# Kernel tuning notes

Measured on AMD Instinct MI355X. Metric: run time of the kernel, lower is better.

The kernel has to match this reference:

```python
import jax, jax.numpy as jnp
import numpy as np

DIM, PATCHES, HID, NCLS, NBLK, PS = 384, 196, 1536, 1000, 24, 16

def fq(w, bits=8):
    # symmetric per-tensor fake quantization (dequantized), as in QAT DynamicQLinear
    n = float(2 ** (bits - 1) - 1)
    s = jnp.max(jnp.abs(w)) / n + 1e-8
    q = jnp.clip(jnp.round(w / s), -n - 1.0, n) * s
    return q

def setup_inputs() -> dict:
    key = jax.random.key(0)
    ks = jax.random.split(key, 12)
    d = {}
    d["x"] = jax.random.normal(ks[0], (64, 3, 224, 224), jnp.float32)
    d["conv_w"] = jax.random.normal(ks[1], (DIM, 3, PS, PS), jnp.float32) * 0.02
    d["conv_b"] = jnp.zeros((DIM,), jnp.float32)
    d["norm1_a"] = jnp.ones((NBLK, DIM), jnp.float32)
    d["norm1_b"] = jnp.zeros((NBLK, DIM), jnp.float32)
    d["attn_w"] = jax.random.normal(ks[2], (NBLK, PATCHES, PATCHES), jnp.float32) * 0.02
    d["attn_b"] = jnp.zeros((NBLK, PATCHES), jnp.float32)
    d["gamma1"] = jnp.full((NBLK, DIM), 1e-4, jnp.float32)
    d["norm2_a"] = jnp.ones((NBLK, DIM), jnp.float32)
    d["norm2_b"] = jnp.zeros((NBLK, DIM), jnp.float32)
    d["mlp_w1"] = jax.random.normal(ks[3], (NBLK, HID, DIM), jnp.float32) * 0.02
    d["mlp_b1"] = jnp.zeros((NBLK, HID), jnp.float32)
    d["mlp_w2"] = jax.random.normal(ks[4], (NBLK, DIM, HID), jnp.float32) * 0.02
    d["mlp_b2"] = jnp.zeros((NBLK, DIM), jnp.float32)
    d["gamma2"] = jnp.full((NBLK, DIM), 1e-4, jnp.float32)
    d["norm_a"] = jnp.ones((DIM,), jnp.float32)
    d["norm_b"] = jnp.zeros((DIM,), jnp.float32)
    d["head_w"] = jax.random.normal(ks[5], (NCLS, DIM), jnp.float32) * 0.02
    d["head_b"] = jnp.zeros((NCLS,), jnp.float32)
    return d

def reference(x, conv_w, conv_b, norm1_a, norm1_b, attn_w, attn_b, gamma1,
              norm2_a, norm2_b, mlp_w1, mlp_b1, mlp_w2, mlp_b2, gamma2,
              norm_a, norm_b, head_w, head_b):
    B = x.shape[0]
    # patch embed: quantized 16x16 stride-16 conv, then flatten(2).transpose(1,2)
    h = jax.lax.conv_general_dilated(x, fq(conv_w), (PS, PS), 'VALID',
                                     dimension_numbers=('NCHW', 'OIHW', 'NCHW'))
    h = h + conv_b[None, :, None, None]
    h = h.reshape(B, DIM, PATCHES).transpose(0, 2, 1)  # [B, 196, 384]

    def step(xc, p):
        a1, b1, aw, ab, g1, a2, b2, w1, bb1, w2, bb2, g2 = p
        # affine norm1 (per-channel)
        t = xc * a1 + b1
        # cross-patch linear applied on transposed layout: out[b,q,d] = sum_p t[b,p,d] W[q,p]
        t = jnp.einsum('bpd,qp->bqd', t, fq(aw)) + ab[None, :, None]
        xc = g1 * t + xc
        # affine norm2 + MLP (384 -> 1536 -> 384, exact GELU)
        t = xc * a2 + b2
        t = jax.nn.gelu(jnp.einsum('bpd,hd->bph', t, fq(w1)) + bb1, approximate=False)
        t = jnp.einsum('bph,dh->bpd', t, fq(w2)) + bb2
        xc = g2 * t + xc
        return xc, None

    h, _ = jax.lax.scan(step, h, (norm1_a, norm1_b, attn_w, attn_b, gamma1,
                                  norm2_a, norm2_b, mlp_w1, mlp_b1, mlp_w2, mlp_b2, gamma2))
    h = h * norm_a + norm_b          # final affine norm
    h = h.mean(axis=1)               # mean pool over patches -> [B, 384]
    return h @ fq(head_w).T + head_b  # [B, 1000]
```

## Files before the change

kernel.cpp:

```cpp
#include <hip/hip_runtime.h>

#define DIM 384
#define PATCHES 196
#define HID 1536
#define NBLK 24
#define NPAD 256
#define XROWS (64 * PATCHES)
#define BDCOLS (64 * DIM)
#define XELEMS (XROWS * DIM)
#define ESTRIDE 132

typedef __attribute__((ext_vector_type(8))) short s8v;
typedef __attribute__((ext_vector_type(4))) float f4v;
typedef unsigned char uchar;
typedef long long i64t;

__device__ __forceinline__ short f2bf(float f) {
  unsigned u = __float_as_uint(f);
  u += 0x7FFFu + ((u >> 16) & 1u);
  return (short)(u >> 16);
}

__device__ __forceinline__ float gelu_f(float x) {
  float u2 = 1.5957691216f * (x + 0.044715f * x * x * x);
  return x / (1.0f + __expf(-u2));
}

__device__ __forceinline__ unsigned pk4_fp8(float a, float b, float c, float d) {
  int lo = __builtin_amdgcn_cvt_pk_fp8_f32(a, b, 0, false);
  int full = __builtin_amdgcn_cvt_pk_fp8_f32(c, d, lo, true);
  return (unsigned)full;
}
__device__ __forceinline__ uchar fp8_1(float a) {
  return (uchar)(__builtin_amdgcn_cvt_pk_fp8_f32(a, a, 0, false) & 0xff);
}

__device__ __forceinline__ void gload_lds16(const void* g, void* l) {
  __builtin_amdgcn_global_load_lds((const __attribute__((address_space(1))) void*)g,
                                   (__attribute__((address_space(3))) void*)l, 16, 0, 0);
}

__global__ __launch_bounds__(256)
void absmax_v4(const float* __restrict__ src, int f4per, int blocks_per,
               unsigned* __restrict__ out) {
  int tens = blockIdx.x / blocks_per;
  int sl = blockIdx.x - tens * blocks_per;
  const float4* p = (const float4*)(src + (size_t)tens * f4per * 4);
  float m = 0.f;
  for (int i = sl * 256 + threadIdx.x; i < f4per; i += blocks_per * 256) {
    float4 v = p[i];
    m = fmaxf(m, fmaxf(fmaxf(fabsf(v.x), fabsf(v.y)), fmaxf(fabsf(v.z), fabsf(v.w))));
  }
  __shared__ float red[256];
  red[threadIdx.x] = m;
  __syncthreads();
  for (int s = 128; s > 0; s >>= 1) {
    if ((int)threadIdx.x < s) red[threadIdx.x] = fmaxf(red[threadIdx.x], red[threadIdx.x + s]);
    __syncthreads();
  }
  if (threadIdx.x == 0) atomicMax(out + tens, __float_as_uint(red[0]));
}

__global__ __launch_bounds__(256)
void quant_w(const float* __restrict__ w, short* __restrict__ q,
             const unsigned* __restrict__ sc, int per, int total) {
  int i = blockIdx.x * 256 + threadIdx.x;
  if (i >= total) return;
  int tens = i / per;
  float s = __uint_as_float(sc[tens]) / 127.0f + 1e-8f;
  float v = rintf(w[i] / s);
  v = fminf(fmaxf(v, -128.0f), 127.0f) * s;
  q[i] = f2bf(v);
}

__global__ __launch_bounds__(256)
void quant_fp8(const float* __restrict__ w, unsigned* __restrict__ q,
               const unsigned* __restrict__ sc, int per, int total4) {
  int i = blockIdx.x * 256 + threadIdx.x;
  if (i >= total4) return;
  int e = i << 2;
  int tens = e / per;
  float s = __uint_as_float(sc[tens]) / 127.0f + 1e-8f;
  float4 w4 = *(const float4*)(w + e);
  float a = fminf(fmaxf(rintf(w4.x / s), -128.0f), 127.0f) * s;
  float b = fminf(fmaxf(rintf(w4.y / s), -128.0f), 127.0f) * s;
  float c = fminf(fmaxf(rintf(w4.z / s), -128.0f), 127.0f) * s;
  float d = fminf(fmaxf(rintf(w4.w / s), -128.0f), 127.0f) * s;
  q[i] = pk4_fp8(a, b, c, d);
}

__global__ __launch_bounds__(256)
void quant_attn_fp8(const float* __restrict__ w, unsigned* __restrict__ q,
                    const unsigned* __restrict__ sc) {
  int i = blockIdx.x * 256 + threadIdx.x;
  if (i >= NBLK * PATCHES * NPAD / 4) return;
  int e = i << 2;
  int col = e & (NPAD - 1);
  int rt = e >> 8;
  int row = rt % PATCHES;
  int tens = rt / PATCHES;
  float s = __uint_as_float(sc[tens]) / 127.0f + 1e-8f;
  const float* wr = w + (size_t)tens * PATCHES * PATCHES + (size_t)row * PATCHES;
  float v[4];
#pragma unroll
  for (int k = 0; k < 4; ++k) {
    int c = col + k;
    v[k] = (c < PATCHES) ? fminf(fmaxf(rintf(wr[c] / s), -128.0f), 127.0f) * s : 0.f;
  }
  q[i] = pk4_fp8(v[0], v[1], v[2], v[3]);
}

__global__ __launch_bounds__(256)
void quant_head_v4(const float* __restrict__ w, float* __restrict__ q,
                   const unsigned* __restrict__ sc) {
  int i = blockIdx.x * 256 + threadIdx.x;
  if (i >= 1000 * DIM / 4) return;
  float s = __uint_as_float(sc[0]) / 127.0f + 1e-8f;
  float4 w4 = *(const float4*)(w + (i << 2));
  float4 o;
  o.x = fminf(fmaxf(rintf(w4.x / s), -128.0f), 127.0f) * s;
  o.y = fminf(fmaxf(rintf(w4.y / s), -128.0f), 127.0f) * s;
  o.z = fminf(fmaxf(rintf(w4.z / s), -128.0f), 127.0f) * s;
  o.w = fminf(fmaxf(rintf(w4.w / s), -128.0f), 127.0f) * s;
  *(float4*)(q + (i << 2)) = o;
}

__global__ __launch_bounds__(256)
void im2col_k(const float* __restrict__ x, short* __restrict__ Xa) {
  int idx = blockIdx.x * 256 + threadIdx.x;
  if (idx >= XROWS * 768 / 4) return;
  int e = idx << 2;
  int r = e / 768, k = e - r * 768;
  int b = r / PATCHES, p = r - b * PATCHES;
  int c = k >> 8, rem = k & 255, ii = rem >> 4, j = rem & 15;
  int ph = p / 14, pw = p - ph * 14;
  const float4 v = *(const float4*)(x + (b * 3 + c) * 50176 + (ph * 16 + ii) * 224 + pw * 16 + j);
  short2* o = (short2*)(Xa + e);
  o[0] = make_short2(f2bf(v.x), f2bf(v.y));
  o[1] = make_short2(f2bf(v.z), f2bf(v.w));
}

__global__ __launch_bounds__(256)
void gemm_conv(const short* __restrict__ A, const short* __restrict__ B,
               float* __restrict__ Xres, const float* __restrict__ bias,
               const float* __restrict__ n1a, const float* __restrict__ n1b,
               uchar* __restrict__ Yt) {
  constexpr int TILE_SHORTS = 192 * 64;
  __shared__ char smem[2 * TILE_SHORTS * 2];
  short* buf0 = (short*)smem;
  float* S = (float*)smem;
  const int lda = 768, K = 768;

  const int t = threadIdx.x;
  const int lane = t & 63;
  const int wid = t >> 6;
  const int wr = wid >> 1, wc = wid & 1;

  const int gx = gridDim.x;
  const int nwg = gx * gridDim.y;
  const int orig = blockIdx.y * gx + blockIdx.x;
  const int q = nwg >> 3, rm = nwg & 7;
  const int xc = orig & 7, jj = orig >> 3;
  const int wg = (xc < rm ? xc * (q + 1) : rm * (q + 1) + (xc - rm) * q) + jj;
  const int bx = wg % gx, by = wg / gx;
  const int m0 = by * 64, n0 = bx * 128;

  f4v acc[2][4];
#pragma unroll
  for (int m = 0; m < 2; ++m)
#pragma unroll
    for (int n = 0; n < 4; ++n) acc[m][n] = (f4v){0.f, 0.f, 0.f, 0.f};

  const int srow = t >> 3;
  const int scol = ((t & 7) ^ (srow & 7)) << 3;
  const short* ga[2];
#pragma unroll
  for (int h = 0; h < 2; ++h) ga[h] = A + (size_t)(m0 + h * 32 + srow) * lda + scol;
  const short* gb[4];
#pragma unroll
  for (int j = 0; j < 4; ++j) gb[j] = B + (size_t)(n0 + j * 32 + srow) * lda + scol;
  short* ldst = buf0 + (t & ~63) * 8;

  auto stage = [&](int slot, int kt) {
    const int koff = kt << 6;
    const int boff = slot * TILE_SHORTS;
    gload_lds16(ga[0] + koff, ldst + boff);
    gload_lds16(ga[1] + koff, ldst + boff + 2048);
#pragma unroll
    for (int j = 0; j < 4; ++j)
      gload_lds16(gb[j] + koff, ldst + boff + 4096 + j * 2048);
  };

  const int l15 = lane & 15, lk = lane >> 4, l7 = lane & 7;
  int paoff[2], pboff[2];
#pragma unroll
  for (int ks = 0; ks < 2; ++ks) {
    const int cgx = ((ks << 2) + lk) ^ l7;
    paoff[ks] = (wr * 32 + l15) * 64 + (cgx << 3);
    pboff[ks] = 4096 + (wc * 64 + l15) * 64 + (cgx << 3);
  }

  const int nk = K >> 6;
  stage(0, 0);
  asm volatile("s_waitcnt vmcnt(0)" ::: "memory");
  __builtin_amdgcn_s_barrier();
  for (int kt = 0; kt < nk; ++kt) {
    const int cur = kt & 1;
    if (kt + 1 < nk) stage(cur ^ 1, kt + 1);
    const short* base = buf0 + cur * TILE_SHORTS;
    s8v af[2][2], bfr[4][2];
#pragma unroll
    for (int m = 0; m < 2; ++m)
#pragma unroll
      for (int ks = 0; ks < 2; ++ks) af[m][ks] = *(const s8v*)(base + paoff[ks] + m * 1024);
#pragma unroll
    for (int n = 0; n < 4; ++n)
#pragma unroll
      for (int ks = 0; ks < 2; ++ks) bfr[n][ks] = *(const s8v*)(base + pboff[ks] + n * 1024);
    asm volatile("s_waitcnt lgkmcnt(0)" ::: "memory");
    __builtin_amdgcn_sched_barrier(0);
    __builtin_amdgcn_s_setprio(1);
#pragma unroll
    for (int m = 0; m < 2; ++m)
#pragma unroll
      for (int n = 0; n < 4; ++n)
#pragma unroll
        for (int ks = 0; ks < 2; ++ks)
          acc[m][n] = __builtin_amdgcn_mfma_f32_16x16x32_bf16(af[m][ks], bfr[n][ks], acc[m][n], 0, 0, 0);
    __builtin_amdgcn_s_setprio(0);
    if (kt + 1 < nk) {
      asm volatile("s_waitcnt vmcnt(0)" ::: "memory");
      __builtin_amdgcn_s_barrier();
    }
  }

  const int cb = (wc << 6) + l15;
  const int rl = t >> 3;
  const int c0 = (t & 7) << 4;
#pragma unroll
  for (int m = 0; m < 2; ++m) {
    __syncthreads();
#pragma unroll
    for (int n = 0; n < 4; ++n) {
      int c = cb + n * 16;
#pragma unroll
      for (int j = 0; j < 4; ++j)
        S[((wr << 4) + (lk << 2) + j) * ESTRIDE + c] = acc[m][n][j];
    }
    __syncthreads();
    const int r = m0 + (rl >> 4) * 32 + m * 16 + (rl & 15);
    const int colg = n0 + c0;
    float xn[16];
#pragma unroll
    for (int i = 0; i < 4; ++i) {
      float4 q4 = *(const float4*)(S + rl * ESTRIDE + c0 + i * 4);
      float4 b4 = *(const float4*)(bias + colg + i * 4);
      float4 o4 = make_float4(q4.x + b4.x, q4.y + b4.y, q4.z + b4.z, q4.w + b4.w);
      *(float4*)(Xres + (size_t)r * DIM + colg + i * 4) = o4;
      xn[4 * i] = o4.x; xn[4 * i + 1] = o4.y; xn[4 * i + 2] = o4.z; xn[4 * i + 3] = o4.w;
    }
    int bb = r / PATCHES, p = r - bb * PATCHES;
    uchar* yrow = Yt + ((size_t)(bb * DIM + colg)) * NPAD + p;
#pragma unroll
    for (int i = 0; i < 4; ++i) {
      float4 a4 = *(const float4*)(n1a + colg + i * 4);
      float4 b4 = *(const float4*)(n1b + colg + i * 4);
      yrow[(4 * i + 0) * NPAD] = fp8_1(xn[4 * i] * a4.x + b4.x);
      yrow[(4 * i + 1) * NPAD] = fp8_1(xn[4 * i + 1] * a4.y + b4.y);
      yrow[(4 * i + 2) * NPAD] = fp8_1(xn[4 * i + 2] * a4.z + b4.z);
      yrow[(4 * i + 3) * NPAD] = fp8_1(xn[4 * i + 3] * a4.w + b4.w);
    }
  }
}

template <int EPI>
__global__ __launch_bounds__(256)
void gemm8(const uchar* __restrict__ A, int lda8, int Mlim,
           const uchar* __restrict__ B, int ldb8, int K,
           float* __restrict__ Xres, uchar* __restrict__ OutB8,
           const float* __restrict__ bias, const float* __restrict__ gamma,
           const float* __restrict__ n2a, const float* __restrict__ n2b,
           const float* __restrict__ n1a, const float* __restrict__ n1b,
           uchar* __restrict__ Yt) {
  constexpr int TILE_BYTES = 192 * 128;
  __shared__ char smem[2 * TILE_BYTES];
  char* buf0 = smem;
  float* S = (float*)smem;

  const int t = threadIdx.x;
  const int lane = t & 63;
  const int wid = t >> 6;
  const int wr = wid >> 1, wc = wid & 1;

  const int gx = gridDim.x;
  const int nwg = gx * gridDim.y;
  const int orig = blockIdx.y * gx + blockIdx.x;
  const int q = nwg >> 3, rm = nwg & 7;
  const int xc = orig & 7, jj = orig >> 3;
  const int wg = (xc < rm ? xc * (q + 1) : rm * (q + 1) + (xc - rm) * q) + jj;
  const int bx = wg % gx, by = wg / gx;
  const int m0 = by * 64, n0 = bx * 128;

  f4v acc[2][4];
#pragma unroll
  for (int m = 0; m < 2; ++m)
#pragma unroll
    for (int n = 0; n < 4; ++n) acc[m][n] = (f4v){0.f, 0.f, 0.f, 0.f};

  const int srow = t >> 3;
  const int scolB = (((t & 7) ^ (srow & 7)) << 4);
  const uchar* ga[2];
#pragma unroll
  for (int h = 0; h < 2; ++h) {
    int r = m0 + h * 32 + srow;
    if (r >= Mlim) r = Mlim - 1;
    ga[h] = A + (size_t)r * lda8 + scolB;
  }
  const uchar* gb[4];
#pragma unroll
  for (int j = 0; j < 4; ++j)
    gb[j] = B + (size_t)(n0 + j * 32 + srow) * ldb8 + scolB;
  char* ldst = buf0 + (t & ~63) * 16;

  auto stage = [&](int slot, int kt) {
    const int koff = kt << 7;
    const int boff = slot * TILE_BYTES;
    gload_lds16(ga[0] + koff, ldst + boff);
    gload_lds16(ga[1] + koff, ldst + boff + 4096);
#pragma unroll
    for (int j = 0; j < 4; ++j)
      gload_lds16(gb[j] + koff, ldst + boff + 8192 + j * 4096);
  };

  const int l15 = lane & 15, lk = lane >> 4, l7 = lane & 7;
  int cterm[4];
#pragma unroll
  for (int ks = 0; ks < 4; ++ks)
    cterm[ks] = ((((ks << 1) + (lk >> 1)) ^ l7) << 4) + ((lk & 1) << 3);
  int arow[2], brow[4];
#pragma unroll
  for (int m = 0; m < 2; ++m) arow[m] = (wr * 32 + m * 16 + l15) << 7;
#pragma unroll
  for (int n = 0; n < 4; ++n) brow[n] = 8192 + ((wc * 64 + n * 16 + l15) << 7);

  const int nk = K >> 7;
  stage(0, 0);
  asm volatile("s_waitcnt vmcnt(0)" ::: "memory");
  __builtin_amdgcn_s_barrier();
  for (int kt = 0; kt < nk; ++kt) {
    const int cur = kt & 1;
    if (kt + 1 < nk) stage(cur ^ 1, kt + 1);
    const char* base = buf0 + cur * TILE_BYTES;
    i64t af[2][4], bfr[4][4];
#pragma unroll
    for (int m = 0; m < 2; ++m)
#pragma unroll
      for (int ks = 0; ks < 4; ++ks) af[m][ks] = *(const i64t*)(base + arow[m] + cterm[ks]);
#pragma unroll
    for (int n = 0; n < 4; ++n)
#pragma unroll
      for (int ks = 0; ks < 4; ++ks) bfr[n][ks] = *(const i64t*)(base + brow[n] + cterm[ks]);
    asm volatile("s_waitcnt lgkmcnt(0)" ::: "memory");
    __builtin_amdgcn_sched_barrier(0);
    __builtin_amdgcn_s_setprio(1);
#pragma unroll
    for (int ks = 0; ks < 4; ++ks)
#pragma unroll
      for (int m = 0; m < 2; ++m)
#pragma unroll
        for (int n = 0; n < 4; ++n)
          acc[m][n] = __builtin_amdgcn_mfma_f32_16x16x32_fp8_fp8(af[m][ks], bfr[n][ks], acc[m][n], 0, 0, 0);
    __builtin_amdgcn_s_setprio(0);
    if (kt + 1 < nk) {
      asm volatile("s_waitcnt vmcnt(0)" ::: "memory");
      __builtin_amdgcn_s_barrier();
    }
  }

  const int cb = (wc << 6) + l15;
  const int rl = t >> 3;
  const int c0 = (t & 7) << 4;
#pragma unroll
  for (int m = 0; m < 2; ++m) {
    __syncthreads();
#pragma unroll
    for (int n = 0; n < 4; ++n) {
      int c = cb + n * 16;
#pragma unroll
      for (int j = 0; j < 4; ++j)
        S[((wr << 4) + (lk << 2) + j) * ESTRIDE + c] = acc[m][n][j];
    }
    __syncthreads();
    const int r = m0 + (rl >> 4) * 32 + m * 16 + (rl & 15);
    const int colg = n0 + c0;
    float v[16];
#pragma unroll
    for (int i = 0; i < 4; ++i) {
      float4 q4 = *(const float4*)(S + rl * ESTRIDE + c0 + i * 4);
      v[4 * i] = q4.x; v[4 * i + 1] = q4.y; v[4 * i + 2] = q4.z; v[4 * i + 3] = q4.w;
    }
    if (EPI == 1) {
      if (r < Mlim) {
        const int b = colg / DIM, d0 = colg - b * DIM;
        const float br = bias[r];
        const size_t base2 = (size_t)b * (PATCHES * DIM) + (size_t)r * DIM + d0;
        float xn[16];
#pragma unroll
        for (int i = 0; i < 4; ++i) {
          float4 g4 = *(const float4*)(gamma + d0 + i * 4);
          float4 x4 = *(const float4*)(Xres + base2 + i * 4);
          x4.x += g4.x * (v[4 * i] + br);
          x4.y += g4.y * (v[4 * i + 1] + br);
          x4.z += g4.z * (v[4 * i + 2] + br);
          x4.w += g4.w * (v[4 * i + 3] + br);
          *(float4*)(Xres + base2 + i * 4) = x4;
          xn[4 * i] = x4.x; xn[4 * i + 1] = x4.y; xn[4 * i + 2] = x4.z; xn[4 * i + 3] = x4.w;
        }
        unsigned o[4];
#pragma unroll
        for (int i = 0; i < 4; ++i) {
          float4 a4 = *(const float4*)(n2a + d0 + i * 4);
          float4 b4 = *(const float4*)(n2b + d0 + i * 4);
          o[i] = pk4_fp8(xn[4 * i] * a4.x + b4.x, xn[4 * i + 1] * a4.y + b4.y,
                         xn[4 * i + 2] * a4.z + b4.z, xn[4 * i + 3] * a4.w + b4.w);
        }
        *(uint4*)(OutB8 + base2) = make_uint4(o[0], o[1], o[2], o[3]);
      }
    } else if (EPI == 2) {
      unsigned o[4];
#pragma unroll
      for (int i = 0; i < 4; ++i) {
        float g0 = gelu_f(v[4 * i] + bias[colg + 4 * i]);
        float g1 = gelu_f(v[4 * i + 1] + bias[colg + 4 * i + 1]);
        float g2 = gelu_f(v[4 * i + 2] + bias[colg + 4 * i + 2]);
        float g3 = gelu_f(v[4 * i + 3] + bias[colg + 4 * i + 3]);
        o[i] = pk4_fp8(g0, g1, g2, g3);
      }
      *(uint4*)(OutB8 + (size_t)r * HID + colg) = make_uint4(o[0], o[1], o[2], o[3]);
    } else {
      float xn[16];
#pragma unroll
      for (int i = 0; i < 4; ++i) {
        float4 b4 = *(const float4*)(bias + colg + i * 4);
        float4 g4 = *(const float4*)(gamma + colg + i * 4);
        float4 x4 = *(const float4*)(Xres + (size_t)r * DIM + colg + i * 4);
        x4.x += g4.x * (v[4 * i] + b4.x);
        x4.y += g4.y * (v[4 * i + 1] + b4.y);
        x4.z += g4.z * (v[4 * i + 2] + b4.z);
        x4.w += g4.w * (v[4 * i + 3] + b4.w);
        *(float4*)(Xres + (size_t)r * DIM + colg + i * 4) = x4;
        xn[4 * i] = x4.x; xn[4 * i + 1] = x4.y; xn[4 * i + 2] = x4.z; xn[4 * i + 3] = x4.w;
      }
      if (Yt != nullptr) {
        int bb = r / PATCHES, p = r - bb * PATCHES;
        uchar* yrow = Yt + ((size_t)(bb * DIM + colg)) * NPAD + p;
#pragma unroll
        for (int i = 0; i < 4; ++i) {
          float4 a4 = *(const float4*)(n1a + colg + i * 4);
          float4 b4 = *(const float4*)(n1b + colg + i * 4);
          yrow[(4 * i + 0) * NPAD] = fp8_1(xn[4 * i] * a4.x + b4.x);
          yrow[(4 * i + 1) * NPAD] = fp8_1(xn[4 * i + 1] * a4.y + b4.y);
          yrow[(4 * i + 2) * NPAD] = fp8_1(xn[4 * i + 2] * a4.z + b4.z);
          yrow[(4 * i + 3) * NPAD] = fp8_1(xn[4 * i + 3] * a4.w + b4.w);
        }
      }
    }
  }
}

__global__ __launch_bounds__(256)
void poolnorm2(const float* __restrict__ X, const float* __restrict__ na,
               const float* __restrict__ nb, float* __restrict__ pooled) {
  __shared__ float red[4][64];
  const int b = blockIdx.x, d0 = blockIdx.y * 64;
  const int dl = threadIdx.x & 63, g = threadIdx.x >> 6;
  const float* p = X + (size_t)b * (PATCHES * DIM) + d0 + dl;
  float s = 0.f;
  for (int i = g; i < PATCHES; i += 4) s += p[(size_t)i * DIM];
  red[g][dl] = s;
  __syncthreads();
  if (threadIdx.x < 64) {
    float tot = red[0][dl] + red[1][dl] + red[2][dl] + red[3][dl];
    int d = d0 + dl;
    pooled[b * DIM + d] = (tot * (1.0f / 196.0f)) * na[d] + nb[d];
  }
}

__global__ __launch_bounds__(256)
void head_k2(const float* __restrict__ pooled, const float* __restrict__ Whq,
             const float* __restrict__ hb, float* __restrict__ out) {
  __shared__ float pl[DIM];
  const int b = blockIdx.x, t = threadIdx.x;
  if (t < 192) {
    pl[t] = pooled[b * DIM + t];
    pl[t + 192] = pooled[b * DIM + t + 192];
  }
  __syncthreads();
  const int n = blockIdx.y * 64 + (t >> 2);
  if (n >= 1000) return;
  const int qofs = (t & 3) * 96;
  const float4* w = (const float4*)(Whq + (size_t)n * DIM + qofs);
  const float* p = pl + qofs;
  float s = 0.f;
#pragma unroll 6
  for (int i = 0; i < 24; ++i) {
    float4 wv = w[i];
    s += p[4 * i] * wv.x + p[4 * i + 1] * wv.y + p[4 * i + 2] * wv.z + p[4 * i + 3] * wv.w;
  }
  s += __shfl_down(s, 2, 4);
  s += __shfl_down(s, 1, 4);
  if ((t & 3) == 0) out[b * 1000 + n] = s + hb[n];
}

extern "C" void kernel_launch(void* const* d_in, const int* in_sizes, int n_in,
                              void* d_out, int out_size, void* d_ws, size_t ws_size,
                              hipStream_t stream) {
  const float* x       = (const float*)d_in[0];
  const float* conv_w  = (const float*)d_in[1];
  const float* conv_b  = (const float*)d_in[2];
  const float* norm1_a = (const float*)d_in[3];
  const float* norm1_b = (const float*)d_in[4];
  const float* attn_w  = (const float*)d_in[5];
  const float* attn_b  = (const float*)d_in[6];
  const float* gamma1  = (const float*)d_in[7];
  const float* norm2_a = (const float*)d_in[8];
  const float* norm2_b = (const float*)d_in[9];
  const float* mlp_w1  = (const float*)d_in[10];
  const float* mlp_b1  = (const float*)d_in[11];
  const float* mlp_w2  = (const float*)d_in[12];
  const float* mlp_b2  = (const float*)d_in[13];
  const float* gamma2  = (const float*)d_in[14];
  const float* norm_a  = (const float*)d_in[15];
  const float* norm_b  = (const float*)d_in[16];
  const float* head_w  = (const float*)d_in[17];
  const float* head_b  = (const float*)d_in[18];
  (void)in_sizes; (void)n_in; (void)out_size; (void)ws_size;

  char* ws = (char*)d_ws;
  size_t off = 0;
  auto alloc = [&](size_t bytes) {
    off = (off + 255) & ~(size_t)255;
    void* p = ws + off;
    off += bytes;
    return p;
  };
  unsigned* scales = (unsigned*)alloc(74 * 4);
  short* conv_wq = (short*)alloc((size_t)DIM * 768 * 2);
  uchar* attn_wq = (uchar*)alloc((size_t)NBLK * PATCHES * NPAD);
  uchar* w1q     = (uchar*)alloc((size_t)NBLK * HID * DIM);
  uchar* w2q     = (uchar*)alloc((size_t)NBLK * DIM * HID);
  float* headq   = (float*)alloc((size_t)1000 * DIM * 4);
  float* X       = (float*)alloc((size_t)XELEMS * 4);
  uchar* Yt      = (uchar*)alloc((size_t)BDCOLS * NPAD);
  uchar* Y2      = (uchar*)alloc((size_t)XELEMS);
  uchar* H       = (uchar*)alloc((size_t)XROWS * HID);
  float* pooled  = (float*)alloc((size_t)64 * DIM * 4);
  short* Xa = (short*)H;

  hipMemsetAsync(scales, 0, 74 * 4, stream);
  hipMemsetAsync(Yt, 0, (size_t)BDCOLS * NPAD, stream);
  absmax_v4<<<32, 256, 0, stream>>>(conv_w, DIM * 768 / 4, 32, scales + 0);
  absmax_v4<<<32, 256, 0, stream>>>(head_w, 1000 * DIM / 4, 32, scales + 1);
  absmax_v4<<<NBLK * 8, 256, 0, stream>>>(attn_w, PATCHES * PATCHES / 4, 8, scales + 2);
  absmax_v4<<<NBLK * 64, 256, 0, stream>>>(mlp_w1, HID * DIM / 4, 64, scales + 26);
  absmax_v4<<<NBLK * 64, 256, 0, stream>>>(mlp_w2, DIM * HID / 4, 64, scales + 50);

  quant_w<<<(DIM * 768 + 255) / 256, 256, 0, stream>>>(conv_w, conv_wq, scales + 0, DIM * 768, DIM * 768);
  quant_fp8<<<(NBLK * HID * DIM / 4 + 255) / 256, 256, 0, stream>>>(
      mlp_w1, (unsigned*)w1q, scales + 26, HID * DIM, NBLK * HID * DIM / 4);
  quant_fp8<<<(NBLK * HID * DIM / 4 + 255) / 256, 256, 0, stream>>>(
      mlp_w2, (unsigned*)w2q, scales + 50, DIM * HID, NBLK * DIM * HID / 4);
  quant_attn_fp8<<<(NBLK * PATCHES * NPAD / 4 + 255) / 256, 256, 0, stream>>>(
      attn_w, (unsigned*)attn_wq, scales + 2);
  quant_head_v4<<<(1000 * DIM / 4 + 255) / 256, 256, 0, stream>>>(head_w, headq, scales + 1);

  im2col_k<<<(XROWS * 768 / 4) / 256, 256, 0, stream>>>(x, Xa);
  gemm_conv<<<dim3(3, 196), 256, 0, stream>>>(Xa, conv_wq, X, conv_b, norm1_a, norm1_b, Yt);

  for (int blk = 0; blk < NBLK; ++blk) {
    gemm8<1><<<dim3(BDCOLS / 128, 4), 256, 0, stream>>>(
        attn_wq + (size_t)blk * PATCHES * NPAD, NPAD, PATCHES, Yt, NPAD, NPAD,
        X, Y2, attn_b + blk * PATCHES, gamma1 + blk * DIM,
        norm2_a + blk * DIM, norm2_b + blk * DIM, nullptr, nullptr, nullptr);
    gemm8<2><<<dim3(HID / 128, XROWS / 64), 256, 0, stream>>>(
        Y2, DIM, XROWS, w1q + (size_t)blk * HID * DIM, DIM, DIM,
        nullptr, H, mlp_b1 + blk * HID, nullptr, nullptr, nullptr,
        nullptr, nullptr, nullptr);
    const bool last = (blk == NBLK - 1);
    gemm8<3><<<dim3(DIM / 128, XROWS / 64), 256, 0, stream>>>(
        H, HID, XROWS, w2q + (size_t)blk * DIM * HID, HID, HID,
        X, nullptr, mlp_b2 + blk * DIM, gamma2 + blk * DIM, nullptr, nullptr,
        last ? nullptr : norm1_a + (blk + 1) * DIM,
        last ? nullptr : norm1_b + (blk + 1) * DIM,
        last ? nullptr : Yt);
  }

  poolnorm2<<<dim3(64, 6), 256, 0, stream>>>(X, norm_a, norm_b, pooled);
  head_k2<<<dim3(64, 16), 256, 0, stream>>>(pooled, headq, head_b, (float*)d_out);
}
```

Measured before the change: 2.130 ms.

## Halve K tile, prefetch two stages ahead, raise occupancy, vectorize epilogue stores

The fp8 GEMM K-tile shrinks from 128 to 64 bytes, which halves LDS use and lets launch_bounds request 4 workgroups per CU. The loop now keeps two stages in flight, waiting with vmcnt(3) instead of draining all loads before each tile. The epilogue stages one 32-row half at a time. The residual-update variant is remapped so each thread owns 4 consecutive patches and writes packed 4-byte fp8 stores into the transposed Yt buffer instead of single-byte scattered stores. The trade-offs are more barriers per K step and more register pressure under the tighter occupancy bound.

```diff
diff --git a/kernel.cpp b/kernel.cpp
--- a/kernel.cpp
+++ b/kernel.cpp
@@ -274,15 +274,15 @@
 }
 
 template <int EPI>
-__global__ __launch_bounds__(256)
-void gemm8(const uchar* __restrict__ A, int lda8, int Mlim,
+__global__ __launch_bounds__(256, 4)
+void gemmS(const uchar* __restrict__ A, int lda8, int Mlim,
            const uchar* __restrict__ B, int ldb8, int K,
            float* __restrict__ Xres, uchar* __restrict__ OutB8,
            const float* __restrict__ bias, const float* __restrict__ gamma,
            const float* __restrict__ n2a, const float* __restrict__ n2b,
            const float* __restrict__ n1a, const float* __restrict__ n1b,
            uchar* __restrict__ Yt) {
-  constexpr int TILE_BYTES = 192 * 128;
+  constexpr int TILE_BYTES = 192 * 64;
   __shared__ char smem[2 * TILE_BYTES];
   char* buf0 = smem;
   float* S = (float*)smem;
@@ -307,161 +307,164 @@
 #pragma unroll
     for (int n = 0; n < 4; ++n) acc[m][n] = (f4v){0.f, 0.f, 0.f, 0.f};
 
-  const int srow = t >> 3;
-  const int scolB = (((t & 7) ^ (srow & 7)) << 4);
-  const uchar* ga[2];
-#pragma unroll
-  for (int h = 0; h < 2; ++h) {
-    int r = m0 + h * 32 + srow;
-    if (r >= Mlim) r = Mlim - 1;
-    ga[h] = A + (size_t)r * lda8 + scolB;
-  }
-  const uchar* gb[4];
-#pragma unroll
-  for (int j = 0; j < 4; ++j)
-    gb[j] = B + (size_t)(n0 + j * 32 + srow) * ldb8 + scolB;
+  const int srow = t >> 2;
+  const int scolB = (((t & 3) ^ (srow & 3)) << 4);
+  int ra = m0 + srow;
+  if (ra >= Mlim) ra = Mlim - 1;
+  const uchar* ga = A + (size_t)ra * lda8 + scolB;
+  const uchar* gb[2];
+#pragma unroll
+  for (int j = 0; j < 2; ++j)
+    gb[j] = B + (size_t)(n0 + j * 64 + srow) * ldb8 + scolB;
   char* ldst = buf0 + (t & ~63) * 16;
 
   auto stage = [&](int slot, int kt) {
-    const int koff = kt << 7;
+    const int koff = kt << 6;
     const int boff = slot * TILE_BYTES;
-    gload_lds16(ga[0] + koff, ldst + boff);
-    gload_lds16(ga[1] + koff, ldst + boff + 4096);
-#pragma unroll
-    for (int j = 0; j < 4; ++j)
-      gload_lds16(gb[j] + koff, ldst + boff + 8192 + j * 4096);
+    gload_lds16(ga + koff, ldst + boff);
+    gload_lds16(gb[0] + koff, ldst + boff + 4096);
+    gload_lds16(gb[1] + koff, ldst + boff + 8192);
   };
 
-  const int l15 = lane & 15, lk = lane >> 4, l7 = lane & 7;
-  int cterm[4];
-#pragma unroll
-  for (int ks = 0; ks < 4; ++ks)
-    cterm[ks] = ((((ks << 1) + (lk >> 1)) ^ l7) << 4) + ((lk & 1) << 3);
+  const int l15 = lane & 15, lk = lane >> 4;
+  int cterm[2];
+#pragma unroll
+  for (int ks = 0; ks < 2; ++ks)
+    cterm[ks] = ((((ks << 1) + (lk >> 1)) ^ (l15 & 3)) << 4) + ((lk & 1) << 3);
   int arow[2], brow[4];
 #pragma unroll
-  for (int m = 0; m < 2; ++m) arow[m] = (wr * 32 + m * 16 + l15) << 7;
-#pragma unroll
-  for (int n = 0; n < 4; ++n) brow[n] = 8192 + ((wc * 64 + n * 16 + l15) << 7);
-
-  const int nk = K >> 7;
+  for (int m = 0; m < 2; ++m) arow[m] = (wr * 32 + m * 16 + l15) << 6;
+#pragma unroll
+  for (int n = 0; n < 4; ++n) brow[n] = 4096 + ((wc * 64 + n * 16 + l15) << 6);
+
+  const int nk = K >> 6;
   stage(0, 0);
-  asm volatile("s_waitcnt vmcnt(0)" ::: "memory");
-  __builtin_amdgcn_s_barrier();
+  if (nk > 1) stage(1, 1);
+  int cur = 0;
   for (int kt = 0; kt < nk; ++kt) {
-    const int cur = kt & 1;
-    if (kt + 1 < nk) stage(cur ^ 1, kt + 1);
+    if (kt + 1 < nk) { asm volatile("s_waitcnt vmcnt(3)" ::: "memory"); }
+    else             { asm volatile("s_waitcnt vmcnt(0)" ::: "memory"); }
+    __builtin_amdgcn_s_barrier();
     const char* base = buf0 + cur * TILE_BYTES;
-    i64t af[2][4], bfr[4][4];
+    i64t af[2][2], bfr[4][2];
 #pragma unroll
     for (int m = 0; m < 2; ++m)
 #pragma unroll
-      for (int ks = 0; ks < 4; ++ks) af[m][ks] = *(const i64t*)(base + arow[m] + cterm[ks]);
+      for (int ks = 0; ks < 2; ++ks) af[m][ks] = *(const i64t*)(base + arow[m] + cterm[ks]);
 #pragma unroll
     for (int n = 0; n < 4; ++n)
 #pragma unroll
-      for (int ks = 0; ks < 4; ++ks) bfr[n][ks] = *(const i64t*)(base + brow[n] + cterm[ks]);
+      for (int ks = 0; ks < 2; ++ks) bfr[n][ks] = *(const i64t*)(base + brow[n] + cterm[ks]);
     asm volatile("s_waitcnt lgkmcnt(0)" ::: "memory");
     __builtin_amdgcn_sched_barrier(0);
     __builtin_amdgcn_s_setprio(1);
 #pragma unroll
-    for (int ks = 0; ks < 4; ++ks)
+    for (int ks = 0; ks < 2; ++ks)
 #pragma unroll
       for (int m = 0; m < 2; ++m)
 #pragma unroll
         for (int n = 0; n < 4; ++n)
           acc[m][n] = __builtin_amdgcn_mfma_f32_16x16x32_fp8_fp8(af[m][ks], bfr[n][ks], acc[m][n], 0, 0, 0);
     __builtin_amdgcn_s_setprio(0);
-    if (kt + 1 < nk) {
-      asm volatile("s_waitcnt vmcnt(0)" ::: "memory");
-      __builtin_amdgcn_s_barrier();
-    }
-  }
-
-  const int cb = (wc << 6) + l15;
-  const int rl = t >> 3;
-  const int c0 = (t & 7) << 4;
-#pragma unroll
-  for (int m = 0; m < 2; ++m) {
+    __builtin_amdgcn_s_barrier();
+    if (kt + 2 < nk) stage(cur, kt + 2);
+    cur ^= 1;
+  }
+
+#pragma unroll
+  for (int hf = 0; hf < 2; ++hf) {
     __syncthreads();
-#pragma unroll
-    for (int n = 0; n < 4; ++n) {
-      int c = cb + n * 16;
-#pragma unroll
-      for (int j = 0; j < 4; ++j)
-        S[((wr << 4) + (lk << 2) + j) * ESTRIDE + c] = acc[m][n][j];
+    if (wr == hf) {
+#pragma unroll
+      for (int m = 0; m < 2; ++m)
+#pragma unroll
+        for (int n = 0; n < 4; ++n) {
+          int srow2 = m * 16 + (lk << 2);
+          int scol2 = wc * 64 + n * 16 + l15;
+#pragma unroll
+          for (int j = 0; j < 4; ++j)
+            S[(srow2 + j) * ESTRIDE + scol2] = acc[m][n][j];
+        }
     }
     __syncthreads();
-    const int r = m0 + (rl >> 4) * 32 + m * 16 + (rl & 15);
-    const int colg = n0 + c0;
-    float v[16];
-#pragma unroll
-    for (int i = 0; i < 4; ++i) {
-      float4 q4 = *(const float4*)(S + rl * ESTRIDE + c0 + i * 4);
-      v[4 * i] = q4.x; v[4 * i + 1] = q4.y; v[4 * i + 2] = q4.z; v[4 * i + 3] = q4.w;
-    }
-    if (EPI == 1) {
-      if (r < Mlim) {
-        const int b = colg / DIM, d0 = colg - b * DIM;
-        const float br = bias[r];
-        const size_t base2 = (size_t)b * (PATCHES * DIM) + (size_t)r * DIM + d0;
-        float xn[16];
+
+    if (EPI == 1 || EPI == 2) {
+      const int rl = t >> 3;
+      const int c0 = (t & 7) << 4;
+      const int r = m0 + hf * 32 + rl;
+      const int colg = n0 + c0;
+      float v[16];
+#pragma unroll
+      for (int i = 0; i < 4; ++i) {
+        float4 q4 = *(const float4*)(S + rl * ESTRIDE + c0 + i * 4);
+        v[4 * i] = q4.x; v[4 * i + 1] = q4.y; v[4 * i + 2] = q4.z; v[4 * i + 3] = q4.w;
+      }
+      if (EPI == 1) {
+        if (r < Mlim) {
+          const int b = colg / DIM, d0 = colg - b * DIM;
+          const float br = bias[r];
+          const size_t base2 = (size_t)b * (PATCHES * DIM) + (size_t)r * DIM + d0;
+          float xn[16];
+#pragma unroll
+          for (int i = 0; i < 4; ++i) {
+            float4 g4 = *(const float4*)(gamma + d0 + i * 4);
+            float4 x4 = *(const float4*)(Xres + base2 + i * 4);
+            x4.x += g4.x * (v[4 * i] + br);
+            x4.y += g4.y * (v[4 * i + 1] + br);
+            x4.z += g4.z * (v[4 * i + 2] + br);
+            x4.w += g4.w * (v[4 * i + 3] + br);
+            *(float4*)(Xres + base2 + i * 4) = x4;
+            xn[4 * i] = x4.x; xn[4 * i + 1] = x4.y; xn[4 * i + 2] = x4.z; xn[4 * i + 3] = x4.w;
+          }
+          unsigned o[4];
+#pragma unroll
+          for (int i = 0; i < 4; ++i) {
+            float4 a4 = *(const float4*)(n2a + d0 + i * 4);
+            float4 b4 = *(const float4*)(n2b + d0 + i * 4);
+            o[i] = pk4_fp8(xn[4 * i] * a4.x + b4.x, xn[4 * i + 1] * a4.y + b4.y,
+                           xn[4 * i + 2] * a4.z + b4.z, xn[4 * i + 3] * a4.w + b4.w);
+          }
+          *(uint4*)(OutB8 + base2) = make_uint4(o[0], o[1], o[2], o[3]);
+        }
+      } else {
+        unsigned o[4];
 #pragma unroll
         for (int i = 0; i < 4; ++i) {
-          float4 g4 = *(const float4*)(gamma + d0 + i * 4);
-          float4 x4 = *(const float4*)(Xres + base2 + i * 4);
-          x4.x += g4.x * (v[4 * i] + br);
-          x4.y += g4.y * (v[4 * i + 1] + br);
-          x4.z += g4.z * (v[4 * i + 2] + br);
-          x4.w += g4.w * (v[4 * i + 3] + br);
-          *(float4*)(Xres + base2 + i * 4) = x4;
-          xn[4 * i] = x4.x; xn[4 * i + 1] = x4.y; xn[4 * i + 2] = x4.z; xn[4 * i + 3] = x4.w;
+          float4 b4 = *(const float4*)(bias + colg + i * 4);
+          o[i] = pk4_fp8(gelu_f(v[4 * i] + b4.x), gelu_f(v[4 * i + 1] + b4.y),
+                         gelu_f(v[4 * i + 2] + b4.z), gelu_f(v[4 * i + 3] + b4.w));
         }
-        unsigned o[4];
-#pragma unroll
-        for (int i = 0; i < 4; ++i) {
-          float4 a4 = *(const float4*)(n2a + d0 + i * 4);
-          float4 b4 = *(const float4*)(n2b + d0 + i * 4);
-          o[i] = pk4_fp8(xn[4 * i] * a4.x + b4.x, xn[4 * i + 1] * a4.y + b4.y,
-                         xn[4 * i + 2] * a4.z + b4.z, xn[4 * i + 3] * a4.w + b4.w);
-        }
-        *(uint4*)(OutB8 + base2) = make_uint4(o[0], o[1], o[2], o[3]);
+        *(uint4*)(OutB8 + (size_t)r * HID + colg) = make_uint4(o[0], o[1], o[2], o[3]);
       }
-    } else if (EPI == 2) {
-      unsigned o[4];
-#pragma unroll
-      for (int i = 0; i < 4; ++i) {
-        float g0 = gelu_f(v[4 * i] + bias[colg + 4 * i]);
-        float g1 = gelu_f(v[4 * i + 1] + bias[colg + 4 * i + 1]);
-        float g2 = gelu_f(v[4 * i + 2] + bias[colg + 4 * i + 2]);
-        float g3 = gelu_f(v[4 * i + 3] + bias[colg + 4 * i + 3]);
-        o[i] = pk4_fp8(g0, g1, g2, g3);
-      }
-      *(uint4*)(OutB8 + (size_t)r * HID + colg) = make_uint4(o[0], o[1], o[2], o[3]);
     } else {
-      float xn[16];
-#pragma unroll
-      for (int i = 0; i < 4; ++i) {
-        float4 b4 = *(const float4*)(bias + colg + i * 4);
-        float4 g4 = *(const float4*)(gamma + colg + i * 4);
-        float4 x4 = *(const float4*)(Xres + (size_t)r * DIM + colg + i * 4);
-        x4.x += g4.x * (v[4 * i] + b4.x);
-        x4.y += g4.y * (v[4 * i + 1] + b4.y);
-        x4.z += g4.z * (v[4 * i + 2] + b4.z);
-        x4.w += g4.w * (v[4 * i + 3] + b4.w);
-        *(float4*)(Xres + (size_t)r * DIM + colg + i * 4) = x4;
-        xn[4 * i] = x4.x; xn[4 * i + 1] = x4.y; xn[4 * i + 2] = x4.z; xn[4 * i + 3] = x4.w;
+      const int r0 = m0 + hf * 32 + ((t & 7) << 2);
+      const int colg = n0 + ((t >> 3) << 2);
+      float4 b4 = *(const float4*)(bias + colg);
+      float4 g4 = *(const float4*)(gamma + colg);
+      float xn[4][4];
+#pragma unroll
+      for (int j = 0; j < 4; ++j) {
+        const int rloc = ((t & 7) << 2) + j;
+        float4 q0 = *(const float4*)(S + rloc * ESTRIDE + (colg - n0));
+        float* xp = Xres + (size_t)(r0 + j) * DIM + colg;
+        float4 x0 = *(const float4*)xp;
+        x0.x += g4.x * (q0.x + b4.x); x0.y += g4.y * (q0.y + b4.y);
+        x0.z += g4.z * (q0.z + b4.z); x0.w += g4.w * (q0.w + b4.w);
+        *(float4*)xp = x0;
+        xn[j][0] = x0.x; xn[j][1] = x0.y; xn[j][2] = x0.z; xn[j][3] = x0.w;
       }
       if (Yt != nullptr) {
-        int bb = r / PATCHES, p = r - bb * PATCHES;
-        uchar* yrow = Yt + ((size_t)(bb * DIM + colg)) * NPAD + p;
+        const int bb = r0 / PATCHES;
+        const int p0 = r0 - bb * PATCHES;
+        float4 a4 = *(const float4*)(n1a + colg);
+        float4 bv4 = *(const float4*)(n1b + colg);
+        float a[4] = {a4.x, a4.y, a4.z, a4.w};
+        float bv[4] = {bv4.x, bv4.y, bv4.z, bv4.w};
 #pragma unroll
         for (int i = 0; i < 4; ++i) {
-          float4 a4 = *(const float4*)(n1a + colg + i * 4);
-          float4 b4 = *(const float4*)(n1b + colg + i * 4);
-          yrow[(4 * i + 0) * NPAD] = fp8_1(xn[4 * i] * a4.x + b4.x);
-          yrow[(4 * i + 1) * NPAD] = fp8_1(xn[4 * i + 1] * a4.y + b4.y);
-          yrow[(4 * i + 2) * NPAD] = fp8_1(xn[4 * i + 2] * a4.z + b4.z);
-          yrow[(4 * i + 3) * NPAD] = fp8_1(xn[4 * i + 3] * a4.w + b4.w);
+          unsigned pk = pk4_fp8(xn[0][i] * a[i] + bv[i], xn[1][i] * a[i] + bv[i],
+                                xn[2][i] * a[i] + bv[i], xn[3][i] * a[i] + bv[i]);
+          *(unsigned*)(Yt + ((size_t)(bb * DIM + colg + i)) * NPAD + p0) = pk;
         }
       }
     }
@@ -578,16 +581,16 @@
   gemm_conv<<<dim3(3, 196), 256, 0, stream>>>(Xa, conv_wq, X, conv_b, norm1_a, norm1_b, Yt);
 
   for (int blk = 0; blk < NBLK; ++blk) {
-    gemm8<1><<<dim3(BDCOLS / 128, 4), 256, 0, stream>>>(
+    gemmS<1><<<dim3(BDCOLS / 128, 4), 256, 0, stream>>>(
         attn_wq + (size_t)blk * PATCHES * NPAD, NPAD, PATCHES, Yt, NPAD, NPAD,
         X, Y2, attn_b + blk * PATCHES, gamma1 + blk * DIM,
         norm2_a + blk * DIM, norm2_b + blk * DIM, nullptr, nullptr, nullptr);
-    gemm8<2><<<dim3(HID / 128, XROWS / 64), 256, 0, stream>>>(
+    gemmS<2><<<dim3(HID / 128, XROWS / 64), 256, 0, stream>>>(
         Y2, DIM, XROWS, w1q + (size_t)blk * HID * DIM, DIM, DIM,
         nullptr, H, mlp_b1 + blk * HID, nullptr, nullptr, nullptr,
         nullptr, nullptr, nullptr);
     const bool last = (blk == NBLK - 1);
-    gemm8<3><<<dim3(DIM / 128, XROWS / 64), 256, 0, stream>>>(
+    gemmS<3><<<dim3(DIM / 128, XROWS / 64), 256, 0, stream>>>(
         H, HID, XROWS, w2q + (size_t)blk * DIM * HID, HID, HID,
         X, nullptr, mlp_b2 + blk * DIM, gamma2 + blk * DIM, nullptr, nullptr,
         last ? nullptr : norm1_a + (blk + 1) * DIM,
```

Measured after the change: 2.262 ms. 1.06x slower.
